# Optimization experiments

Measured on AMD Instinct MI355X. Metric: run time of the kernel, lower is better.

The kernel has to match this reference:

```python
import jax, jax.numpy as jnp
import numpy as np

COUPLING = 1.0
DT = 1.0
ATTRACTION = 1.0
EPS = 1e-6


def setup_inputs() -> dict:
    key = jax.random.key(0)
    k1, k2, k3, k4 = jax.random.split(key, 4)
    B, N, D = 4, 2048, 4
    theta_prev = jax.random.normal(k1, (B, N, D), dtype=jnp.float32)
    gamma_prev = jax.random.normal(k2, (B, N, D), dtype=jnp.float32)
    theta_connectivity_weight = jax.random.uniform(k3, (B, N, N), dtype=jnp.float32)
    alpha_t = jax.random.normal(k4, (B, N, N), dtype=jnp.float32)
    return {
        "theta_prev": theta_prev,
        "gamma_prev": gamma_prev,
        "theta_connectivity_weight": theta_connectivity_weight,
        "alpha_t": alpha_t,
    }


def reference(theta_prev, gamma_prev, theta_connectivity_weight, alpha_t):
    # Pairwise coupling: coupling/N * sum_j W[b,i,j] * sin(theta[b,j,d] - theta[b,i,d] - alpha[b,i,j])
    # Expanded via trig identities so the O(N^2*D) tensor is never materialized:
    #   sin(tj - ti - a) = cos(a)*(s_j c_i - c_j s_i) - sin(a)*(c_j c_i + s_j s_i)
    # => sum_j W_ij sin(...) = c_i*(A s)_i - s_i*(A c)_i - c_i*(Bm c)_i - s_i*(Bm s)_i
    # with A = W*cos(alpha), Bm = W*sin(alpha). This matches the chunked torch loop exactly.
    n = theta_prev.shape[1]
    s = jnp.sin(theta_prev)  # [B, N, D]
    c = jnp.cos(theta_prev)  # [B, N, D]
    A = theta_connectivity_weight * jnp.cos(alpha_t)   # [B, N, N]
    Bm = theta_connectivity_weight * jnp.sin(alpha_t)  # [B, N, N]
    As = jnp.einsum("bij,bjd->bid", A, s)
    Ac = jnp.einsum("bij,bjd->bid", A, c)
    Bs = jnp.einsum("bij,bjd->bid", Bm, s)
    Bc = jnp.einsum("bij,bjd->bid", Bm, c)
    coupling_term = (COUPLING / n) * (c * As - s * Ac - c * Bc - s * Bs)
    drive_term = ATTRACTION * (gamma_prev - theta_prev)
    theta_next = theta_prev + DT * (drive_term + coupling_term)
    # torch F.normalize: x / clamp(||x||_2, min=eps) along last dim
    norm = jnp.linalg.norm(theta_next, axis=-1, keepdims=True)
    return theta_next / jnp.maximum(norm, EPS)
```

## Files before the change

### kernel.cpp

```cpp
#include <hip/hip_runtime.h>
#include <stdint.h>

#define N_NODES 2048
#define N_BATCH 4
#define ROWS_PER_BLOCK 8
#define THREADS 512
#define NTILES (N_NODES / 256)

__device__ __forceinline__ uint32_t bf16rn(float x) {
    uint32_t u = __float_as_uint(x);
    u += 0x7fffu + ((u >> 16) & 1u);
    return u >> 16;
}

__global__ __launch_bounds__(THREADS, 4) void kuramoto_kernel(
    const float* __restrict__ theta,
    const float* __restrict__ gamma,
    const float* __restrict__ W,
    const float* __restrict__ alpha,
    float* __restrict__ out)
{
    __shared__ uint32_t tbl[4][N_NODES];

    const int tid  = threadIdx.x;
    const int lane = tid & 63;
    const int wave = tid >> 6;
    const int b    = blockIdx.x >> 8;
    const int i    = ((blockIdx.x & 255) * ROWS_PER_BLOCK) + wave;

    const size_t rowbase = ((size_t)b * N_NODES + i) * N_NODES;
    const float* Wr = W + rowbase;
    const float* Ar = alpha + rowbase;

    float4 wrow[NTILES], arow[NTILES];
    #pragma unroll
    for (int k = 0; k < NTILES; ++k) {
        const int j0 = k * 256 + lane * 4;
        wrow[k] = *(const float4*)(Wr + j0);
        arow[k] = *(const float4*)(Ar + j0);
    }

    const float* thb = theta + (size_t)b * (N_NODES * 4);
    #pragma unroll
    for (int g = 0; g < N_NODES / THREADS; ++g) {
        const int j = tid + g * THREADS;
        const float4 u = *(const float4*)(thb + (size_t)j * 4);
        const float th[4] = {u.x, u.y, u.z, u.w};
        #pragma unroll
        for (int d = 0; d < 4; ++d) {
            float s, c;
            __sincosf(th[d], &s, &c);
            tbl[d][j] = (bf16rn(c) << 16) | bf16rn(s);
        }
    }
    __syncthreads();

    float re[4] = {0.f, 0.f, 0.f, 0.f};
    float im[4] = {0.f, 0.f, 0.f, 0.f};

    #pragma unroll
    for (int k = 0; k < NTILES; ++k) {
        const int j0 = k * 256 + lane * 4;
        const float wq[4] = {wrow[k].x, wrow[k].y, wrow[k].z, wrow[k].w};
        const float aq[4] = {arow[k].x, arow[k].y, arow[k].z, arow[k].w};
        float A[4], Bq[4];
        #pragma unroll
        for (int q = 0; q < 4; ++q) {
            float sa, ca;
            __sincosf(aq[q], &sa, &ca);
            A[q]  = wq[q] * ca;
            Bq[q] = wq[q] * sa;
        }
        #pragma unroll
        for (int d = 0; d < 4; ++d) {
            const uint4 t = *(const uint4*)&tbl[d][j0];
            const uint32_t tu[4] = {t.x, t.y, t.z, t.w};
            #pragma unroll
            for (int q = 0; q < 4; ++q) {
                const float s = __uint_as_float(tu[q] << 16);
                const float c = __uint_as_float(tu[q] & 0xffff0000u);
                re[d] = fmaf(A[q],   c, re[d]);
                re[d] = fmaf(Bq[q],  s, re[d]);
                im[d] = fmaf(A[q],   s, im[d]);
                im[d] = fmaf(-Bq[q], c, im[d]);
            }
        }
    }

    #pragma unroll
    for (int stage = 1; stage < 64; stage <<= 1) {
        #pragma unroll
        for (int d = 0; d < 4; ++d) {
            re[d] += __shfl_xor(re[d], stage, 64);
            im[d] += __shfl_xor(im[d], stage, 64);
        }
    }

    if (lane == 0) {
        const size_t obase = ((size_t)b * N_NODES + i) * 4;
        const float4 th4 = *(const float4*)(thb + (size_t)i * 4);
        const float4 g4  = *(const float4*)(gamma + obase);
        const float thd[4] = {th4.x, th4.y, th4.z, th4.w};
        const float gd[4]  = {g4.x, g4.y, g4.z, g4.w};
        float t[4];
        float s2 = 0.0f;
        #pragma unroll
        for (int d = 0; d < 4; ++d) {
            float s_i, c_i;
            __sincosf(thd[d], &s_i, &c_i);
            const float coup = (c_i * im[d] - s_i * re[d]) * (1.0f / (float)N_NODES);
            t[d] = gd[d] + coup;
            s2 = fmaf(t[d], t[d], s2);
        }
        const float inv = 1.0f / fmaxf(sqrtf(s2), 1e-6f);
        *(float4*)(out + obase) = make_float4(t[0]*inv, t[1]*inv, t[2]*inv, t[3]*inv);
    }
}

extern "C" void kernel_launch(void* const* d_in, const int* in_sizes, int n_in,
                              void* d_out, int out_size, void* d_ws, size_t ws_size,
                              hipStream_t stream) {
    const float* theta = (const float*)d_in[0];
    const float* gamma = (const float*)d_in[1];
    const float* W     = (const float*)d_in[2];
    const float* alpha = (const float*)d_in[3];
    float* out = (float*)d_out;

    const int grid = (N_BATCH * N_NODES) / ROWS_PER_BLOCK;
    hipLaunchKernelGGL(kuramoto_kernel, dim3(grid), dim3(THREADS), 0, stream,
                       theta, gamma, W, alpha, out);
}
```

Baseline: 151.0 us.

## Stream W and alpha rows through LDS with double-buffered async global-to-LDS loads

```diff
diff --git a/kernel.cpp b/kernel.cpp
--- a/kernel.cpp
+++ b/kernel.cpp
@@ -5,13 +5,24 @@
 #define N_BATCH 4
 #define ROWS_PER_BLOCK 8
 #define THREADS 512
-#define NTILES (N_NODES / 256)
+#define TJ 256
+#define NTILES (N_NODES / TJ)
 
 __device__ __forceinline__ uint32_t bf16rn(float x) {
     uint32_t u = __float_as_uint(x);
     u += 0x7fffu + ((u >> 16) & 1u);
     return u >> 16;
 }
+
+__device__ __forceinline__ void gload_lds16(const float* g, float* l) {
+    __builtin_amdgcn_global_load_lds(
+        (const __attribute__((address_space(1))) void*)(g),
+        (__attribute__((address_space(3))) void*)(l),
+        16, 0, 0);
+}
+
+#define WAITV(N)  asm volatile("s_waitcnt vmcnt(" #N ")" ::: "memory")
+#define WAITLGKM0 asm volatile("s_waitcnt lgkmcnt(0)" ::: "memory")
 
 __global__ __launch_bounds__(THREADS, 4) void kuramoto_kernel(
     const float* __restrict__ theta,
@@ -21,6 +32,7 @@
     float* __restrict__ out)
 {
     __shared__ uint32_t tbl[4][N_NODES];
+    __shared__ float stg[ROWS_PER_BLOCK][2][2][TJ];
 
     const int tid  = threadIdx.x;
     const int lane = tid & 63;
@@ -32,13 +44,10 @@
     const float* Wr = W + rowbase;
     const float* Ar = alpha + rowbase;
 
-    float4 wrow[NTILES], arow[NTILES];
-    #pragma unroll
-    for (int k = 0; k < NTILES; ++k) {
-        const int j0 = k * 256 + lane * 4;
-        wrow[k] = *(const float4*)(Wr + j0);
-        arow[k] = *(const float4*)(Ar + j0);
-    }
+    gload_lds16(Wr + 0      + lane * 4, &stg[wave][0][0][0]);
+    gload_lds16(Ar + 0      + lane * 4, &stg[wave][0][1][0]);
+    gload_lds16(Wr + TJ     + lane * 4, &stg[wave][1][0][0]);
+    gload_lds16(Ar + TJ     + lane * 4, &stg[wave][1][1][0]);
 
     const float* thb = theta + (size_t)b * (N_NODES * 4);
     #pragma unroll
@@ -60,9 +69,24 @@
 
     #pragma unroll
     for (int k = 0; k < NTILES; ++k) {
-        const int j0 = k * 256 + lane * 4;
-        const float wq[4] = {wrow[k].x, wrow[k].y, wrow[k].z, wrow[k].w};
-        const float aq[4] = {arow[k].x, arow[k].y, arow[k].z, arow[k].w};
+        if (k < NTILES - 1) { WAITV(2); } else { WAITV(0); }
+        __builtin_amdgcn_sched_barrier(0);
+
+        const int buf = k & 1;
+        const float4 wv = *(const float4*)&stg[wave][buf][0][lane * 4];
+        const float4 av = *(const float4*)&stg[wave][buf][1][lane * 4];
+        WAITLGKM0;
+        __builtin_amdgcn_sched_barrier(0);
+
+        if (k + 2 < NTILES) {
+            const int jn = (k + 2) * TJ + lane * 4;
+            gload_lds16(Wr + jn, &stg[wave][buf][0][0]);
+            gload_lds16(Ar + jn, &stg[wave][buf][1][0]);
+        }
+
+        const int j0 = k * TJ + lane * 4;
+        const float wq[4] = {wv.x, wv.y, wv.z, wv.w};
+        const float aq[4] = {av.x, av.y, av.z, av.w};
         float A[4], Bq[4];
         #pragma unroll
         for (int q = 0; q < 4; ++q) {
```

After: 153.0 us. No clear change (+1.3%).
